# Optimization experiments

Hardware: AMD Instinct MI355X
Metric: run time of the kernel (lower is better)

Reference implementation:

```python
import jax, jax.numpy as jnp
import numpy as np

EPS = 1e-5
CROSS = 12  # cross_size


def bn(x, g, b):
    # inference BatchNorm2d with running_mean=0, running_var=1
    s = g / jnp.sqrt(1.0 + EPS)
    return x * s[None, :, None, None] + b[None, :, None, None]


def conv1x1(x, w, b=None):
    # w: [out_c, in_c]
    y = jnp.einsum('bchw,oc->bohw', x, w)
    if b is not None:
        y = y + b[None, :, None, None]
    return y


def mlp(x, w1, b1, w2, b2):
    # Mlp with channels_first=True: 1x1 conv -> GELU -> 1x1 conv (drop=0)
    return conv1x1(jax.nn.gelu(conv1x1(x, w1, b1), approximate=False), w2, b2)


def setup_inputs() -> dict:
    key = jax.random.key(0)
    ks = jax.random.split(key, 24)
    B, Cl, Ch = 8, 128, 64
    Hl = Wl = 96
    Hh = Wh = 192

    def w(k, o, i):
        return jax.random.normal(k, (o, i), jnp.float32) / np.float32(np.sqrt(i))

    return {
        'x_l': jax.random.normal(ks[0], (B, Cl, Hl, Wl), jnp.float32),
        'x_h': jax.random.normal(ks[1], (B, Ch, Hh, Wh), jnp.float32),
        # mlp_l (hidden = in = Cl)
        'mlp_l_w1': w(ks[2], Cl, Cl), 'mlp_l_b1': jnp.zeros((Cl,), jnp.float32),
        'mlp_l_w2': w(ks[3], Cl, Cl), 'mlp_l_b2': jnp.zeros((Cl,), jnp.float32),
        # conv_1x1(Cl->Ch) + BN + ReLU
        'conv_w': w(ks[4], Ch, Cl),
        'conv_bn_g': jnp.ones((Ch,), jnp.float32), 'conv_bn_b': jnp.zeros((Ch,), jnp.float32),
        # cross_kv: BN(Cl) -> AdaptiveMaxPool(12,12) -> Conv1x1(Cl -> 2*Ch)
        'kv_bn_g': jnp.ones((Cl,), jnp.float32), 'kv_bn_b': jnp.zeros((Cl,), jnp.float32),
        'kv_w': w(ks[5], 2 * Ch, Cl), 'kv_b': jnp.zeros((2 * Ch,), jnp.float32),
        # self.norm: BN(Ch)
        'norm_g': jnp.ones((Ch,), jnp.float32), 'norm_b': jnp.zeros((Ch,), jnp.float32),
        # mlp_h
        'mlp_h_w1': w(ks[6], Ch, Ch), 'mlp_h_b1': jnp.zeros((Ch,), jnp.float32),
        'mlp_h_w2': w(ks[7], Ch, Ch), 'mlp_h_b2': jnp.zeros((Ch,), jnp.float32),
    }


def reference(x_l, x_h,
              mlp_l_w1, mlp_l_b1, mlp_l_w2, mlp_l_b2,
              conv_w, conv_bn_g, conv_bn_b,
              kv_bn_g, kv_bn_b, kv_w, kv_b,
              norm_g, norm_b,
              mlp_h_w1, mlp_h_b1, mlp_h_w2, mlp_h_b2):
    B, Cl, Hl, Wl = x_l.shape
    _, Ch, Hh, Wh = x_h.shape
    S = CROSS * CROSS  # 144

    # x_l = x_l + mlp_l(x_l)
    x_l = x_l + mlp(x_l, mlp_l_w1, mlp_l_b1, mlp_l_w2, mlp_l_b2)

    # x_h = x_h + interpolate(conv(x_l))
    x_l_conv = jax.nn.relu(bn(conv1x1(x_l, conv_w), conv_bn_g, conv_bn_b))
    up = jax.image.resize(x_l_conv, (B, Ch, Hh, Wh), method='linear')
    x_h = x_h + up

    # cross_kv(x_l): BN -> adaptive max pool to 12x12 -> 1x1 conv to 2*Ch
    xn_l = bn(x_l, kv_bn_g, kv_bn_b)
    pooled = xn_l.reshape(B, Cl, CROSS, Hl // CROSS, CROSS, Wl // CROSS).max(axis=(3, 5))
    kv = conv1x1(pooled, kv_w, kv_b)              # [B, 2*Ch, 12, 12]
    k, v = kv[:, :Ch], kv[:, Ch:]                 # each [B, Ch, 12, 12]
    k_mat = k.transpose(0, 2, 3, 1).reshape(B, S, Ch)  # grouped-conv kernel [B,S,Ch]
    v_mat = v.reshape(B, Ch, S)                        # grouped-conv kernel [B,Ch,S]

    # attn_h
    xn_h = bn(x_h, norm_g, norm_b)                # [B,Ch,Hh,Wh]
    attn = jnp.einsum('bchw,bsc->bshw', xn_h, k_mat)  # [B,S,Hh,Wh]
    attn = jax.nn.softmax(attn * (S ** -0.5), axis=1)
    out = jnp.einsum('bshw,bcs->bchw', attn, v_mat)   # [B,Ch,Hh,Wh]
    x_h = x_h + out

    # x_h = x_h + mlp_h(x_h)
    x_h = x_h + mlp(x_h, mlp_h_w1, mlp_h_b1, mlp_h_w2, mlp_h_b2)
    return x_h
```

## Files before the change

### kernel.cpp

```cpp
#include <hip/hip_runtime.h>
#include <math.h>

#define NB 8
#define CL 128
#define CH 64
#define HL 96
#define WL 96
#define PL (HL*WL)
#define HH 192
#define WH 192
#define PH (HH*WH)
#define NS 144
#define BN_S 0.9999950000374997f
#define INV12 (1.0f/12.0f)

typedef __attribute__((ext_vector_type(8))) short bf16x8;
typedef __attribute__((ext_vector_type(4))) float f32x4;
#define MFMA16(a,b,c) __builtin_amdgcn_mfma_f32_16x16x32_bf16(a,b,c,0,0,0)

__device__ __forceinline__ float gelu_exact(float x){
    return 0.5f*x*(1.0f + erff(x*0.7071067811865475f));
}
__device__ __forceinline__ short f2bf(float f){
    union { float f; unsigned u; } v; v.f = f;
    unsigned r = v.u + 0x7FFFu + ((v.u >> 16) & 1u);
    return (short)(r >> 16);
}

__global__ __launch_bounds__(256) void k_mlp_l(
    const float* __restrict__ xl, const float* __restrict__ w1, const float* __restrict__ b1,
    const float* __restrict__ w2, const float* __restrict__ b2, float* __restrict__ xl2)
{
    __shared__ short Wb[128*136];
    __shared__ short Xb[64*136];
    __shared__ float bS[256];
    const int tid = threadIdx.x;
    const int b   = blockIdx.x / (PL/64);
    const int hw0 = (blockIdx.x % (PL/64)) * 64;
    const float* xb = xl + (size_t)b*CL*PL + hw0;
    #pragma unroll
    for (int i=0;i<64;i++){ int idx=i*256+tid; Wb[(idx>>7)*136 + (idx&127)] = f2bf(w1[idx]); }
    #pragma unroll
    for (int i=0;i<32;i++){ int idx=i*256+tid; int c=idx>>6, p=idx&63;
        Xb[p*136+c] = f2bf(xb[(size_t)c*PL + p]); }
    if (tid < 128) bS[tid] = b1[tid]; else bS[tid] = b2[tid-128];
    __syncthreads();
    const int w = tid>>6, lane = tid&63, l16 = lane&15, q = lane>>4;
    const int pw = w*16;
    float hv[8][4];
    #pragma unroll
    for (int mt=0; mt<8; mt++){
        f32x4 acc = {0.f,0.f,0.f,0.f};
        #pragma unroll
        for (int k=0;k<4;k++){
            bf16x8 af = *(const bf16x8*)&Wb[(mt*16+l16)*136 + k*32 + q*8];
            bf16x8 bf = *(const bf16x8*)&Xb[(pw+l16)*136 + k*32 + q*8];
            acc = MFMA16(af, bf, acc);
        }
        #pragma unroll
        for (int r=0;r<4;r++) hv[mt][r] = gelu_exact(acc[r] + bS[mt*16+q*4+r]);
    }
    #pragma unroll
    for (int mt=0;mt<8;mt++)
        #pragma unroll
        for (int r=0;r<4;r++)
            Xb[(pw+l16)*136 + mt*16+q*4+r] = f2bf(hv[mt][r]);
    __syncthreads();
    #pragma unroll
    for (int i=0;i<64;i++){ int idx=i*256+tid; Wb[(idx>>7)*136 + (idx&127)] = f2bf(w2[idx]); }
    __syncthreads();
    float* yb = xl2 + (size_t)b*CL*PL + hw0;
    #pragma unroll
    for (int mt=0; mt<8; mt++){
        f32x4 acc = {0.f,0.f,0.f,0.f};
        #pragma unroll
        for (int k=0;k<4;k++){
            bf16x8 af = *(const bf16x8*)&Wb[(mt*16+l16)*136 + k*32 + q*8];
            bf16x8 bf = *(const bf16x8*)&Xb[(pw+l16)*136 + k*32 + q*8];
            acc = MFMA16(af, bf, acc);
        }
        #pragma unroll
        for (int r=0;r<4;r++){
            int o = mt*16 + q*4 + r;
            size_t off = (size_t)o*PL + pw + l16;
            yb[off] = acc[r] + bS[128+o] + xb[off];
        }
    }
}

__global__ __launch_bounds__(256) void k_conv_l(
    const float* __restrict__ xl2, const float* __restrict__ cw,
    const float* __restrict__ bng, const float* __restrict__ bnb, float* __restrict__ xc)
{
    __shared__ short Wb[64*136];
    __shared__ short Xb[64*136];
    const int tid = threadIdx.x;
    const int b   = blockIdx.x / (PL/64);
    const int hw0 = (blockIdx.x % (PL/64)) * 64;
    const float* xb = xl2 + (size_t)b*CL*PL + hw0;
    #pragma unroll
    for (int i=0;i<32;i++){ int idx=i*256+tid; Wb[(idx>>7)*136 + (idx&127)] = f2bf(cw[idx]); }
    #pragma unroll
    for (int i=0;i<32;i++){ int idx=i*256+tid; int c=idx>>6, p=idx&63;
        Xb[p*136+c] = f2bf(xb[(size_t)c*PL + p]); }
    __syncthreads();
    const int w = tid>>6, lane = tid&63, l16 = lane&15, q = lane>>4;
    const int pw = w*16;
    float* yb = xc + (size_t)b*CH*PL + hw0;
    #pragma unroll
    for (int mt=0; mt<4; mt++){
        f32x4 acc = {0.f,0.f,0.f,0.f};
        #pragma unroll
        for (int k=0;k<4;k++){
            bf16x8 af = *(const bf16x8*)&Wb[(mt*16+l16)*136 + k*32 + q*8];
            bf16x8 bf = *(const bf16x8*)&Xb[(pw+l16)*136 + k*32 + q*8];
            acc = MFMA16(af, bf, acc);
        }
        #pragma unroll
        for (int r=0;r<4;r++){
            int o = mt*16 + q*4 + r;
            float sc = bng[o]*BN_S, bb = bnb[o];
            yb[(size_t)o*PL + pw + l16] = fmaxf(sc*acc[r] + bb, 0.f);
        }
    }
}

__global__ __launch_bounds__(192) void k_pool(
    const float* __restrict__ xl2, const float* __restrict__ g, const float* __restrict__ bta,
    float* __restrict__ pooled)
{
    const int plane = blockIdx.x;
    const int tid = threadIdx.x;
    if (tid >= NS) return;
    const int c = plane & (CL-1);
    const float sc = g[c]*BN_S;
    const float tc = bta[c];
    const int i = tid/12, j = tid%12;
    const float* base = xl2 + (size_t)plane*PL + (size_t)i*8*WL + j*8;
    float m = -3.4e38f;
    #pragma unroll
    for (int dy=0;dy<8;dy++){
        const float* rr = base + dy*WL;
        #pragma unroll
        for (int dx=0;dx<8;dx++) m = fmaxf(m, sc*rr[dx]+tc);
    }
    pooled[(size_t)plane*NS + tid] = m;
}

__global__ __launch_bounds__(256) void k_kv(
    const float* __restrict__ pooled, const float* __restrict__ kvw, const float* __restrict__ kvb,
    const float* __restrict__ ng, const float* __restrict__ nb,
    float* __restrict__ keg, float* __restrict__ vg, float* __restrict__ biasg)
{
    const int t = blockIdx.x*256 + threadIdx.x;
    const int s = t % NS;
    const int r = t / NS;
    const int o = r & 127;
    const int b = r >> 7;
    const float* P = pooled + (size_t)b*CL*NS + s;
    const float* W = kvw + (size_t)o*CL;
    float acc = kvb[o];
    #pragma unroll 4
    for (int c=0;c<CL;c++) acc = fmaf(W[c], P[(size_t)c*NS], acc);
    if (o < CH){
        keg[((size_t)b*NS+s)*CH + o] = acc * (ng[o]*(BN_S*INV12));
        atomicAdd(&biasg[b*NS+s], acc * (nb[o]*INV12));
    } else {
        vg[((size_t)b*NS+s)*CH + (o-CH)] = acc;
    }
}

__global__ __launch_bounds__(256) void k_attn(
    const float* __restrict__ xh, const float* __restrict__ xc,
    const float* __restrict__ keg, const float* __restrict__ vg,
    const float* __restrict__ biasg, float* __restrict__ out)
{
    __shared__ short KVb[64*168];
    __shared__ short Xb[64*72];
    __shared__ short Pt[64*168];
    __shared__ float bS[NS];
    const int tid = threadIdx.x;
    const int b   = blockIdx.x / (PH/64);
    const int hw0 = (blockIdx.x % (PH/64)) * 64;
    const int y   = hw0 / WH;
    const int xst = hw0 % WH;
    const int   lyr = (y>>1) - ((y&1)^1);
    const float fy  = (y&1) ? 0.25f : 0.75f;
    const int   y0i = lyr<0?0:lyr;
    const int   y1i = (lyr+1>HL-1)?(HL-1):(lyr+1);

    const float* xb  = xh + (size_t)b*CH*PH + hw0;
    const float* xcb = xc + (size_t)b*CH*PL;
    const float* keb = keg + (size_t)b*NS*CH;
    #pragma unroll
    for (int i=0;i<36;i++){ int idx=i*256+tid; KVb[(idx>>6)*72 + (idx&63)] = f2bf(keb[idx]); }
    #pragma unroll
    for (int i=0;i<16;i++){
        int idx=i*256+tid; int c=idx>>6, p=idx&63;
        int xo = xst + p;
        int lx = (xo>>1) - ((xo&1)^1);
        float fx = (xo&1) ? 0.25f : 0.75f;
        int x0i = lx<0?0:lx; int x1i = (lx+1>WL-1)?(WL-1):(lx+1);
        const float* s = xcb + (size_t)c*PL;
        float v00 = s[y0i*WL+x0i], v01 = s[y0i*WL+x1i];
        float v10 = s[y1i*WL+x0i], v11 = s[y1i*WL+x1i];
        float top = v00 + fx*(v01-v00);
        float bot = v10 + fx*(v11-v10);
        float up  = top + fy*(bot-top);
        Xb[p*72+c] = f2bf(xb[(size_t)c*PH + p] + up);
    }
    if (tid < NS) bS[tid] = biasg[b*NS+tid];
    #pragma unroll
    for (int i=0;i<4;i++){ int idx=i*256+tid; Pt[(idx>>4)*168 + 144 + (idx&15)] = 0; }
    __syncthreads();
    const int w = tid>>6, lane = tid&63, l16 = lane&15, q = lane>>4;
    const int pw = w*16;
    float ev[9][4];
    float mloc = -3.4e38f;
    #pragma unroll
    for (int st=0; st<9; st++){
        f32x4 acc = {0.f,0.f,0.f,0.f};
        #pragma unroll
        for (int k=0;k<2;k++){
            bf16x8 af = *(const bf16x8*)&KVb[(st*16+l16)*72 + k*32 + q*8];
            bf16x8 bf = *(const bf16x8*)&Xb[(pw+l16)*72 + k*32 + q*8];
            acc = MFMA16(af, bf, acc);
        }
        #pragma unroll
        for (int r=0;r<4;r++){
            float v = acc[r] + bS[st*16+q*4+r];
            ev[st][r] = v; mloc = fmaxf(mloc, v);
        }
    }
    mloc = fmaxf(mloc, __shfl_xor(mloc,16));
    mloc = fmaxf(mloc, __shfl_xor(mloc,32));
    float sloc = 0.f;
    #pragma unroll
    for (int st=0;st<9;st++)
        #pragma unroll
        for (int r=0;r<4;r++){ float e = __expf(ev[st][r]-mloc); ev[st][r]=e; sloc+=e; }
    sloc += __shfl_xor(sloc,16);
    sloc += __shfl_xor(sloc,32);
    const float rs = 1.f/sloc;
    #pragma unroll
    for (int st=0;st<9;st++)
        #pragma unroll
        for (int r=0;r<4;r++)
            Pt[(pw+l16)*168 + st*16+q*4+r] = f2bf(ev[st][r]);
    __syncthreads();
    const float* vb = vg + (size_t)b*NS*CH;
    #pragma unroll
    for (int i=0;i<36;i++){ int idx=i*256+tid; int s=idx>>6, c=idx&63;
        KVb[c*168 + s] = f2bf(vb[idx]); }
    #pragma unroll
    for (int i=0;i<4;i++){ int idx=i*256+tid; KVb[(idx>>4)*168 + 144 + (idx&15)] = 0; }
    __syncthreads();
    float* ob = out + (size_t)b*CH*PH + hw0;
    const int px  = pw + l16;
    const int xo  = xst + px;
    const int lxe = (xo>>1) - ((xo&1)^1);
    const float fxe = (xo&1) ? 0.25f : 0.75f;
    const int x0e = lxe<0?0:lxe;
    const int x1e = (lxe+1>WL-1)?(WL-1):(lxe+1);
    #pragma unroll
    for (int mt=0; mt<4; mt++){
        f32x4 acc = {0.f,0.f,0.f,0.f};
        #pragma unroll
        for (int k=0;k<5;k++){
            bf16x8 af = *(const bf16x8*)&KVb[(mt*16+l16)*168 + k*32 + q*8];
            bf16x8 bf = *(const bf16x8*)&Pt[(pw+l16)*168 + k*32 + q*8];
            acc = MFMA16(af, bf, acc);
        }
        #pragma unroll
        for (int r=0;r<4;r++){
            int ch = mt*16 + q*4 + r;
            const float* s = xcb + (size_t)ch*PL;
            float v00 = s[y0i*WL+x0e], v01 = s[y0i*WL+x1e];
            float v10 = s[y1i*WL+x0e], v11 = s[y1i*WL+x1e];
            float top = v00 + fxe*(v01-v00);
            float bot = v10 + fxe*(v11-v10);
            float up  = top + fy*(bot-top);
            size_t off = (size_t)ch*PH + px;
            ob[off] = (xb[off] + up) + acc[r]*rs;
        }
    }
}

__global__ __launch_bounds__(256) void k_mlp_h(
    float* __restrict__ xh, const float* __restrict__ w1, const float* __restrict__ b1,
    const float* __restrict__ w2, const float* __restrict__ b2)
{
    __shared__ short Wb[64*72];
    __shared__ short Xb[64*72];
    __shared__ float bS[128];
    const int tid = threadIdx.x;
    const int b   = blockIdx.x / (PH/64);
    const int hw0 = (blockIdx.x % (PH/64)) * 64;
    float* xb = xh + (size_t)b*CH*PH + hw0;
    #pragma unroll
    for (int i=0;i<16;i++){ int idx=i*256+tid; Wb[(idx>>6)*72 + (idx&63)] = f2bf(w1[idx]); }
    #pragma unroll
    for (int i=0;i<16;i++){ int idx=i*256+tid; int c=idx>>6, p=idx&63;
        Xb[p*72+c] = f2bf(xb[(size_t)c*PH + p]); }
    if (tid < 64) bS[tid] = b1[tid]; else if (tid < 128) bS[tid] = b2[tid-64];
    __syncthreads();
    const int w = tid>>6, lane = tid&63, l16 = lane&15, q = lane>>4;
    const int pw = w*16;
    float hv[4][4];
    #pragma unroll
    for (int mt=0; mt<4; mt++){
        f32x4 acc = {0.f,0.f,0.f,0.f};
        #pragma unroll
        for (int k=0;k<2;k++){
            bf16x8 af = *(const bf16x8*)&Wb[(mt*16+l16)*72 + k*32 + q*8];
            bf16x8 bf = *(const bf16x8*)&Xb[(pw+l16)*72 + k*32 + q*8];
            acc = MFMA16(af, bf, acc);
        }
        #pragma unroll
        for (int r=0;r<4;r++) hv[mt][r] = gelu_exact(acc[r] + bS[mt*16+q*4+r]);
    }
    #pragma unroll
    for (int mt=0;mt<4;mt++)
        #pragma unroll
        for (int r=0;r<4;r++)
            Xb[(pw+l16)*72 + mt*16+q*4+r] = f2bf(hv[mt][r]);
    __syncthreads();
    #pragma unroll
    for (int i=0;i<16;i++){ int idx=i*256+tid; Wb[(idx>>6)*72 + (idx&63)] = f2bf(w2[idx]); }
    __syncthreads();
    #pragma unroll
    for (int mt=0; mt<4; mt++){
        f32x4 acc = {0.f,0.f,0.f,0.f};
        #pragma unroll
        for (int k=0;k<2;k++){
            bf16x8 af = *(const bf16x8*)&Wb[(mt*16+l16)*72 + k*32 + q*8];
            bf16x8 bf = *(const bf16x8*)&Xb[(pw+l16)*72 + k*32 + q*8];
            acc = MFMA16(af, bf, acc);
        }
        #pragma unroll
        for (int r=0;r<4;r++){
            int o = mt*16 + q*4 + r;
            size_t off = (size_t)o*PH + pw + l16;
            xb[off] = acc[r] + bS[64+o] + xb[off];
        }
    }
}

extern "C" void kernel_launch(void* const* d_in, const int* in_sizes, int n_in,
                              void* d_out, int out_size, void* d_ws, size_t ws_size,
                              hipStream_t stream)
{
    const float* xl    = (const float*)d_in[0];
    const float* xh    = (const float*)d_in[1];
    const float* ml_w1 = (const float*)d_in[2];
    const float* ml_b1 = (const float*)d_in[3];
    const float* ml_w2 = (const float*)d_in[4];
    const float* ml_b2 = (const float*)d_in[5];
    const float* cw    = (const float*)d_in[6];
    const float* cbg   = (const float*)d_in[7];
    const float* cbb   = (const float*)d_in[8];
    const float* kbg   = (const float*)d_in[9];
    const float* kbb   = (const float*)d_in[10];
    const float* kvw   = (const float*)d_in[11];
    const float* kvb   = (const float*)d_in[12];
    const float* ng    = (const float*)d_in[13];
    const float* nb    = (const float*)d_in[14];
    const float* mh_w1 = (const float*)d_in[15];
    const float* mh_b1 = (const float*)d_in[16];
    const float* mh_w2 = (const float*)d_in[17];
    const float* mh_b2 = (const float*)d_in[18];
    float* out = (float*)d_out;

    float* ws     = (float*)d_ws;
    float* xl2    = ws;
    float* xc     = xl2    + (size_t)NB*CL*PL;
    float* pooled = xc     + (size_t)NB*CH*PL;
    float* keg    = pooled + (size_t)NB*CL*NS;
    float* vg     = keg    + (size_t)NB*NS*CH;
    float* biasg  = vg     + (size_t)NB*NS*CH;

    k_mlp_l<<<dim3(NB*PL/64), dim3(256), 0, stream>>>(xl, ml_w1, ml_b1, ml_w2, ml_b2, xl2);
    k_conv_l<<<dim3(NB*PL/64), dim3(256), 0, stream>>>(xl2, cw, cbg, cbb, xc);
    k_pool<<<dim3(NB*CL), dim3(192), 0, stream>>>(xl2, kbg, kbb, pooled);
    hipMemsetAsync(biasg, 0, (size_t)NB*NS*sizeof(float), stream);
    k_kv<<<dim3((NB*128*NS)/256), dim3(256), 0, stream>>>(pooled, kvw, kvb, ng, nb, keg, vg, biasg);
    k_attn<<<dim3(NB*PH/64), dim3(256), 0, stream>>>(xh, xc, keg, vg, biasg, out);
    k_mlp_h<<<dim3(NB*PH/64), dim3(256), 0, stream>>>(out, mh_w1, mh_b1, mh_w2, mh_b2);
}
```

Baseline: 357.6 us.

## Fuse mlp_h into the attention kernel, keeping the residual in registers

The separate k_mlp_h kernel is removed and its two 1x1 convs with GELU now run at the end of k_attn. The post-attention residual stays in registers, and the MLP weights are staged into the free Pt shared buffer. This is meant to remove a full write and re-read of the high-resolution x_h tensor, plus one kernel launch. The upsample and x_h loads are also moved to the start so each value is read once. In exchange, per-thread register pressure in k_attn rises (resid[16] alongside ev[9][4]), which could lower occupancy.

```diff
diff --git a/kernel.cpp b/kernel.cpp
--- a/kernel.cpp
+++ b/kernel.cpp
@@ -173,12 +173,16 @@
 __global__ __launch_bounds__(256) void k_attn(
     const float* __restrict__ xh, const float* __restrict__ xc,
     const float* __restrict__ keg, const float* __restrict__ vg,
-    const float* __restrict__ biasg, float* __restrict__ out)
+    const float* __restrict__ biasg,
+    const float* __restrict__ w1h, const float* __restrict__ b1h,
+    const float* __restrict__ w2h, const float* __restrict__ b2h,
+    float* __restrict__ out)
 {
     __shared__ short KVb[64*168];
     __shared__ short Xb[64*72];
     __shared__ short Pt[64*168];
     __shared__ float bS[NS];
+    __shared__ float bH[128];
     const int tid = threadIdx.x;
     const int b   = blockIdx.x / (PH/64);
     const int hw0 = (blockIdx.x % (PH/64)) * 64;
@@ -192,29 +196,41 @@
     const float* xb  = xh + (size_t)b*CH*PH + hw0;
     const float* xcb = xc + (size_t)b*CH*PL;
     const float* keb = keg + (size_t)b*NS*CH;
-    #pragma unroll
-    for (int i=0;i<36;i++){ int idx=i*256+tid; KVb[(idx>>6)*72 + (idx&63)] = f2bf(keb[idx]); }
-    #pragma unroll
-    for (int i=0;i<16;i++){
-        int idx=i*256+tid; int c=idx>>6, p=idx&63;
-        int xo = xst + p;
-        int lx = (xo>>1) - ((xo&1)^1);
-        float fx = (xo&1) ? 0.25f : 0.75f;
-        int x0i = lx<0?0:lx; int x1i = (lx+1>WL-1)?(WL-1):(lx+1);
-        const float* s = xcb + (size_t)c*PL;
-        float v00 = s[y0i*WL+x0i], v01 = s[y0i*WL+x1i];
-        float v10 = s[y1i*WL+x0i], v11 = s[y1i*WL+x1i];
-        float top = v00 + fx*(v01-v00);
-        float bot = v10 + fx*(v11-v10);
-        float up  = top + fy*(bot-top);
-        Xb[p*72+c] = f2bf(xb[(size_t)c*PH + p] + up);
-    }
-    if (tid < NS) bS[tid] = biasg[b*NS+tid];
-    #pragma unroll
-    for (int i=0;i<4;i++){ int idx=i*256+tid; Pt[(idx>>4)*168 + 144 + (idx&15)] = 0; }
-    __syncthreads();
+
     const int w = tid>>6, lane = tid&63, l16 = lane&15, q = lane>>4;
     const int pw = w*16;
+    const int px = pw + l16;
+
+    #pragma unroll
+    for (int i=0;i<36;i++){ int idx=i*256+tid; KVb[(idx>>6)*72 + (idx&63)] = f2bf(keb[idx]); }
+    if (tid < NS) bS[tid] = biasg[b*NS+tid];
+    if (tid < 64) bH[tid] = b1h[tid]; else if (tid < 128) bH[tid] = b2h[tid-64];
+    #pragma unroll
+    for (int i=0;i<4;i++){ int idx=i*256+tid; Pt[(idx>>4)*168 + 144 + (idx&15)] = 0; }
+
+    const int xo  = xst + px;
+    const int lx  = (xo>>1) - ((xo&1)^1);
+    const float fx = (xo&1) ? 0.25f : 0.75f;
+    const int x0i = lx<0?0:lx;
+    const int x1i = (lx+1>WL-1)?(WL-1):(lx+1);
+    float resid[16];
+    #pragma unroll
+    for (int mt=0; mt<4; mt++)
+        #pragma unroll
+        for (int r=0; r<4; r++){
+            int ch = mt*16 + q*4 + r;
+            const float* s = xcb + (size_t)ch*PL;
+            float v00 = s[y0i*WL+x0i], v01 = s[y0i*WL+x1i];
+            float v10 = s[y1i*WL+x0i], v11 = s[y1i*WL+x1i];
+            float top = v00 + fx*(v01-v00);
+            float bot = v10 + fx*(v11-v10);
+            float up  = top + fy*(bot-top);
+            float val = xb[(size_t)ch*PH + px] + up;
+            resid[mt*4+r] = val;
+            Xb[px*72+ch] = f2bf(val);
+        }
+    __syncthreads();
+
     float ev[9][4];
     float mloc = -3.4e38f;
     #pragma unroll
@@ -255,13 +271,7 @@
     #pragma unroll
     for (int i=0;i<4;i++){ int idx=i*256+tid; KVb[(idx>>4)*168 + 144 + (idx&15)] = 0; }
     __syncthreads();
-    float* ob = out + (size_t)b*CH*PH + hw0;
-    const int px  = pw + l16;
-    const int xo  = xst + px;
-    const int lxe = (xo>>1) - ((xo&1)^1);
-    const float fxe = (xo&1) ? 0.25f : 0.75f;
-    const int x0e = lxe<0?0:lxe;
-    const int x1e = (lxe+1>WL-1)?(WL-1):(lxe+1);
+
     #pragma unroll
     for (int mt=0; mt<4; mt++){
         f32x4 acc = {0.f,0.f,0.f,0.f};
@@ -273,75 +283,51 @@
         }
         #pragma unroll
         for (int r=0;r<4;r++){
+            float v = resid[mt*4+r] + acc[r]*rs;
+            resid[mt*4+r] = v;
+            Xb[px*72 + mt*16+q*4+r] = f2bf(v);
+        }
+    }
+    __syncthreads();
+    #pragma unroll
+    for (int i=0;i<16;i++){ int idx=i*256+tid; Pt[(idx>>6)*168 + (idx&63)] = f2bf(w1h[idx]); }
+    #pragma unroll
+    for (int i=0;i<16;i++){ int idx=i*256+tid; Pt[(idx>>6)*168 + 72 + (idx&63)] = f2bf(w2h[idx]); }
+    __syncthreads();
+
+    float hv[4][4];
+    #pragma unroll
+    for (int mt=0; mt<4; mt++){
+        f32x4 acc = {0.f,0.f,0.f,0.f};
+        #pragma unroll
+        for (int k=0;k<2;k++){
+            bf16x8 af = *(const bf16x8*)&Pt[(mt*16+l16)*168 + k*32 + q*8];
+            bf16x8 bf = *(const bf16x8*)&Xb[(pw+l16)*72 + k*32 + q*8];
+            acc = MFMA16(af, bf, acc);
+        }
+        #pragma unroll
+        for (int r=0;r<4;r++) hv[mt][r] = gelu_exact(acc[r] + bH[mt*16+q*4+r]);
+    }
+    #pragma unroll
+    for (int mt=0;mt<4;mt++)
+        #pragma unroll
+        for (int r=0;r<4;r++)
+            Xb[px*72 + mt*16+q*4+r] = f2bf(hv[mt][r]);
+
+    float* ob = out + (size_t)b*CH*PH + hw0;
+    #pragma unroll
+    for (int mt=0; mt<4; mt++){
+        f32x4 acc = {0.f,0.f,0.f,0.f};
+        #pragma unroll
+        for (int k=0;k<2;k++){
+            bf16x8 af = *(const bf16x8*)&Pt[(mt*16+l16)*168 + 72 + k*32 + q*8];
+            bf16x8 bf = *(const bf16x8*)&Xb[(pw+l16)*72 + k*32 + q*8];
+            acc = MFMA16(af, bf, acc);
+        }
+        #pragma unroll
+        for (int r=0;r<4;r++){
             int ch = mt*16 + q*4 + r;
-            const float* s = xcb + (size_t)ch*PL;
-            float v00 = s[y0i*WL+x0e], v01 = s[y0i*WL+x1e];
-            float v10 = s[y1i*WL+x0e], v11 = s[y1i*WL+x1e];
-            float top = v00 + fxe*(v01-v00);
-            float bot = v10 + fxe*(v11-v10);
-            float up  = top + fy*(bot-top);
-            size_t off = (size_t)ch*PH + px;
-            ob[off] = (xb[off] + up) + acc[r]*rs;
-        }
-    }
-}
-
-__global__ __launch_bounds__(256) void k_mlp_h(
-    float* __restrict__ xh, const float* __restrict__ w1, const float* __restrict__ b1,
-    const float* __restrict__ w2, const float* __restrict__ b2)
-{
-    __shared__ short Wb[64*72];
-    __shared__ short Xb[64*72];
-    __shared__ float bS[128];
-    const int tid = threadIdx.x;
-    const int b   = blockIdx.x / (PH/64);
-    const int hw0 = (blockIdx.x % (PH/64)) * 64;
-    float* xb = xh + (size_t)b*CH*PH + hw0;
-    #pragma unroll
-    for (int i=0;i<16;i++){ int idx=i*256+tid; Wb[(idx>>6)*72 + (idx&63)] = f2bf(w1[idx]); }
-    #pragma unroll
-    for (int i=0;i<16;i++){ int idx=i*256+tid; int c=idx>>6, p=idx&63;
-        Xb[p*72+c] = f2bf(xb[(size_t)c*PH + p]); }
-    if (tid < 64) bS[tid] = b1[tid]; else if (tid < 128) bS[tid] = b2[tid-64];
-    __syncthreads();
-    const int w = tid>>6, lane = tid&63, l16 = lane&15, q = lane>>4;
-    const int pw = w*16;
-    float hv[4][4];
-    #pragma unroll
-    for (int mt=0; mt<4; mt++){
-        f32x4 acc = {0.f,0.f,0.f,0.f};
-        #pragma unroll
-        for (int k=0;k<2;k++){
-            bf16x8 af = *(const bf16x8*)&Wb[(mt*16+l16)*72 + k*32 + q*8];
-            bf16x8 bf = *(const bf16x8*)&Xb[(pw+l16)*72 + k*32 + q*8];
-            acc = MFMA16(af, bf, acc);
-        }
-        #pragma unroll
-        for (int r=0;r<4;r++) hv[mt][r] = gelu_exact(acc[r] + bS[mt*16+q*4+r]);
-    }
-    #pragma unroll
-    for (int mt=0;mt<4;mt++)
-        #pragma unroll
-        for (int r=0;r<4;r++)
-            Xb[(pw+l16)*72 + mt*16+q*4+r] = f2bf(hv[mt][r]);
-    __syncthreads();
-    #pragma unroll
-    for (int i=0;i<16;i++){ int idx=i*256+tid; Wb[(idx>>6)*72 + (idx&63)] = f2bf(w2[idx]); }
-    __syncthreads();
-    #pragma unroll
-    for (int mt=0; mt<4; mt++){
-        f32x4 acc = {0.f,0.f,0.f,0.f};
-        #pragma unroll
-        for (int k=0;k<2;k++){
-            bf16x8 af = *(const bf16x8*)&Wb[(mt*16+l16)*72 + k*32 + q*8];
-            bf16x8 bf = *(const bf16x8*)&Xb[(pw+l16)*72 + k*32 + q*8];
-            acc = MFMA16(af, bf, acc);
-        }
-        #pragma unroll
-        for (int r=0;r<4;r++){
-            int o = mt*16 + q*4 + r;
-            size_t off = (size_t)o*PH + pw + l16;
-            xb[off] = acc[r] + bS[64+o] + xb[off];
+            ob[(size_t)ch*PH + px] = acc[r] + bH[64+ch] + resid[mt*4+r];
         }
     }
 }
@@ -384,6 +370,6 @@
     k_pool<<<dim3(NB*CL), dim3(192), 0, stream>>>(xl2, kbg, kbb, pooled);
     hipMemsetAsync(biasg, 0, (size_t)NB*NS*sizeof(float), stream);
     k_kv<<<dim3((NB*128*NS)/256), dim3(256), 0, stream>>>(pooled, kvw, kvb, ng, nb, keg, vg, biasg);
-    k_attn<<<dim3(NB*PH/64), dim3(256), 0, stream>>>(xh, xc, keg, vg, biasg, out);
-    k_mlp_h<<<dim3(NB*PH/64), dim3(256), 0, stream>>>(out, mh_w1, mh_b1, mh_w2, mh_b2);
-}
+    k_attn<<<dim3(NB*PH/64), dim3(256), 0, stream>>>(xh, xc, keg, vg, biasg,
+                                                     mh_w1, mh_b1, mh_w2, mh_b2, out);
+}
```

Result: faster. 337.4 us (-5.7%).
